# Performance work log

Hardware: AMD Instinct MI355X
Metric: run time of the kernel (lower is better)

## Reference

```python
import jax, jax.numpy as jnp
import numpy as np

EPS = 1e-05
BITW = 8
BITA = 8


def _ste_round(v):
    # round with identity gradient (TF Round->Identity override)
    return v + jax.lax.stop_gradient(jnp.round(v) - v)


def _quantize_overflow(x, bits):
    # tensorlayer _quantize_overflow: linear quantization over [min, max]
    n = 2.0 ** bits - 1.0
    mx = jnp.max(x)
    mn = jnp.min(x)
    step = jax.lax.stop_gradient((mx - mn) / n)
    return _ste_round((x - mn) / step) * step + mn


def _conv2d_same(x, w):
    # x: [N,H,W,C], w: [KH,KW,C,F]
    return jax.lax.conv_general_dilated(
        x, w, window_strides=(1, 1), padding='SAME',
        dimension_numbers=('NHWC', 'HWIO', 'NHWC'))


def setup_inputs() -> dict:
    key = jax.random.key(0)
    k1, k2 = jax.random.split(key)
    x = jax.random.normal(k1, (32, 56, 56, 128), dtype=jnp.float32)
    W = jax.random.normal(k2, (3, 3, 128, 256), dtype=jnp.float32) * 0.02
    gamma = jnp.ones((256,), dtype=jnp.float32)
    beta = jnp.zeros((256,), dtype=jnp.float32)
    return {"x": x, "W": W, "gamma": gamma, "beta": beta}


def reference(x, W, gamma, beta):
    # 1) fake-quantize activations
    xq = _quantize_overflow(x, BITA)
    # 2) full-precision conv to get batch statistics (training path)
    conv_out = _conv2d_same(x, W)  # [N,H,W,F]
    mean = jnp.mean(conv_out, axis=(0, 1, 2))          # [F]
    var = jnp.var(conv_out, axis=(0, 1, 2))            # [F], biased (tf.nn.moments)
    inv_std = 1.0 / jnp.sqrt(var + EPS)                # [F]
    # 3) fold BN into weights/bias
    w_fold = W * (gamma * inv_std)                     # broadcast over [KH,KW,C,F]
    bias_fold = beta - gamma * mean * inv_std          # [F]
    # 4) quantize folded weights, conv with quantized activations
    wq = _quantize_overflow(w_fold, BITW)
    out = _conv2d_same(xq, wq) + bias_fold
    return jax.nn.relu(out)
```

## Files before the change

### kernel.cpp

```cpp
#include <hip/hip_runtime.h>

typedef float f32x4_t __attribute__((ext_vector_type(4)));
typedef __bf16 bf16x8_t __attribute__((ext_vector_type(8)));
typedef unsigned short u16x8_t __attribute__((ext_vector_type(8)));

#define NPIX        100352
#define PIX_PER_IMG 3136
#define PH          58
#define PPIX        3364
#define C_IN        128
#define C_OUT       256
#define NTAPS       9
#define NV4         3211264
#define NWELEM      294912
#define MTILES      392
#define NPADPIX     107648

#define OFF_ENC     0
#define OFF_SCALE   64
#define OFF_BIAS    1152
#define OFF_WT      4096
#define OFF_WQT     593920
#define OFF_PSUM    1183744
#define OFF_PSQ     1986560
#define OFF_XPAD    2789376
#define OFF_XQPAD   30347264

__device__ __forceinline__ unsigned short f2bf(float x) {
  unsigned u = __float_as_uint(x);
  u += 0x7FFFu + ((u >> 16) & 1u);
  return (unsigned short)(u >> 16);
}
__device__ __forceinline__ unsigned encf(float v) {
  unsigned u = __float_as_uint(v);
  return (u & 0x80000000u) ? ~u : (u | 0x80000000u);
}
__device__ __forceinline__ float decf(unsigned e) {
  unsigned u = (e & 0x80000000u) ? (e ^ 0x80000000u) : ~e;
  return __uint_as_float(u);
}
__device__ __forceinline__ void gl_lds16(const void* g, void* l) {
  auto gp = (const __attribute__((address_space(1))) unsigned*)(const unsigned*)g;
  auto lp = (__attribute__((address_space(3))) unsigned*)(unsigned*)l;
  __builtin_amdgcn_global_load_lds(gp, lp, 16, 0, 0);
}
#define SCHED_FENCE() __builtin_amdgcn_sched_barrier(0)

__global__ void kinit(unsigned* enc) {
  enc[0] = 0xFFFFFFFFu;
  enc[1] = 0u;
  enc[2] = 0xFFFFFFFFu;
  enc[3] = 0u;
}

__global__ void kminmax(const float4* __restrict__ x, unsigned* __restrict__ enc) {
  const int tid = blockIdx.x * blockDim.x + threadIdx.x;
  const int stride = gridDim.x * blockDim.x;
  float mn = 3.4e38f, mx = -3.4e38f;
  for (int i = tid; i < NV4; i += stride) {
    float4 v = x[i];
    mn = fminf(mn, fminf(fminf(v.x, v.y), fminf(v.z, v.w)));
    mx = fmaxf(mx, fmaxf(fmaxf(v.x, v.y), fmaxf(v.z, v.w)));
  }
  #pragma unroll
  for (int off = 32; off > 0; off >>= 1) {
    mn = fminf(mn, __shfl_xor(mn, off));
    mx = fmaxf(mx, __shfl_xor(mx, off));
  }
  __shared__ float smn[4], smx[4];
  const int lane = threadIdx.x & 63, w = threadIdx.x >> 6;
  if (lane == 0) { smn[w] = mn; smx[w] = mx; }
  __syncthreads();
  if (threadIdx.x == 0) {
    mn = fminf(fminf(smn[0], smn[1]), fminf(smn[2], smn[3]));
    mx = fmaxf(fmaxf(smx[0], smx[1]), fmaxf(smx[2], smx[3]));
    atomicMin(&enc[0], encf(mn));
    atomicMax(&enc[1], encf(mx));
  }
}

__global__ void kwconv(const float* __restrict__ W, unsigned short* __restrict__ wt) {
  const int idx = blockIdx.x * 256 + threadIdx.x;
  if (idx >= NWELEM) return;
  const int c = idx & 127;
  const int f = (idx >> 7) & 255;
  const int tap = idx >> 15;
  wt[idx] = f2bf(W[(tap * 128 + c) * 256 + f]);
}

__global__ void kwq(const float* __restrict__ W, const float* __restrict__ scale,
                    const unsigned* __restrict__ enc, unsigned short* __restrict__ wqt) {
  const int idx = blockIdx.x * 256 + threadIdx.x;
  if (idx >= NWELEM) return;
  const int c = idx & 127;
  const int f = (idx >> 7) & 255;
  const int tap = idx >> 15;
  const float wmn = decf(enc[2]), wmx = decf(enc[3]);
  const float wstep = (wmx - wmn) / 255.0f;
  const float wrstep = 255.0f / (wmx - wmn);
  const float v = W[(tap * 128 + c) * 256 + f] * scale[f];
  const float q = rintf((v - wmn) * wrstep) * wstep + wmn;
  wqt[idx] = f2bf(q);
}

__global__ void kpadfill(const float* __restrict__ x, const unsigned* __restrict__ enc,
                         unsigned short* __restrict__ xpad, unsigned short* __restrict__ xqpad)
{
  const int tid = blockIdx.x * 256 + threadIdx.x;
  if (tid >= NPADPIX * 16) return;
  const int pp = tid >> 4;
  const int c8 = (tid & 15) << 3;
  const int n = pp / PPIX;
  const int rem = pp - n * PPIX;
  const int hp = rem / PH;
  const int wp = rem - hp * PH;
  u16x8_t vb, vq;
  #pragma unroll
  for (int j = 0; j < 8; ++j) { vb[j] = 0; vq[j] = 0; }
  if (hp >= 1 && hp <= 56 && wp >= 1 && wp <= 56) {
    const float mn = decf(enc[0]), mx = decf(enc[1]);
    const float step = (mx - mn) / 255.0f, rstep = 255.0f / (mx - mn);
    const float* src = x + ((n * PIX_PER_IMG) + (hp - 1) * 56 + (wp - 1)) * C_IN + c8;
    const float4 a = *(const float4*)src;
    const float4 b = *(const float4*)(src + 4);
    const float v[8] = {a.x, a.y, a.z, a.w, b.x, b.y, b.z, b.w};
    #pragma unroll
    for (int j = 0; j < 8; ++j) {
      vb[j] = f2bf(v[j]);
      const float qv = rintf((v[j] - mn) * rstep) * step + mn;
      vq[j] = f2bf(qv);
    }
  }
  *(u16x8_t*)(xpad + pp * C_IN + c8) = vb;
  *(u16x8_t*)(xqpad + pp * C_IN + c8) = vq;
}

template<int STATS>
__global__ __launch_bounds__(512, 4)
void kconv(const unsigned short* __restrict__ xin,
           const unsigned short* __restrict__ wt,
           float* __restrict__ out,
           const float* __restrict__ bias,
           float* __restrict__ psum,
           float* __restrict__ psq)
{
  const int bid = blockIdx.x;
  const int slot = (bid & 7) * 98 + (bid >> 3);
  const int bm = slot >> 1;
  const int bn = slot & 1;

  const int tid = threadIdx.x;
  const int lane = tid & 63;
  const int wid = tid >> 6;
  const int wm = wid >> 1;
  const int wn = wid & 1;
  const int l16 = lane & 15;
  const int rsub = lane >> 4;

  __shared__ __align__(16) unsigned char smem[49152];

  unsigned aoff[2];
  {
    const int arow0 = wid * 8 + (lane >> 3);
    const int pc = lane & 7;
    #pragma unroll
    for (int j = 0; j < 2; ++j) {
      const int row = j * 64 + arow0;
      const int lc = pc ^ (row & 7);
      const int pix = bm * 256 + row + 128 * (lc >> 2);
      const int n = pix / PIX_PER_IMG;
      const int rem = pix - n * PIX_PER_IMG;
      const int hh = rem / 56;
      const int ww = rem - hh * 56;
      aoff[j] = (unsigned)((n * PPIX + hh * PH + ww) * C_IN + (lc & 3) * 8);
    }
  }
  unsigned boff;
  {
    const int row = wid * 8 + (lane >> 3);
    const int pc = lane & 7;
    const int lc = pc ^ (row & 7);
    const int f = bn * 128 + row + 64 * (lc >> 2);
    boff = (unsigned)(f * C_IN + (lc & 3) * 8);
  }

  int a_rd[4], b_rd[4];
  #pragma unroll
  for (int im = 0; im < 4; ++im) {
    const int p = wm * 64 + im * 16 + l16;
    const int row = p & 127, half = p >> 7;
    const int phys = (half * 4 + rsub) ^ (row & 7);
    a_rd[im] = row * 128 + phys * 16;
  }
  #pragma unroll
  for (int in = 0; in < 4; ++in) {
    const int f = wn * 64 + in * 16 + l16;
    const int row = f & 63, half = f >> 6;
    const int phys = (half * 4 + rsub) ^ (row & 7);
    b_rd[in] = row * 128 + phys * 16;
  }

  f32x4_t acc[4][4];
  #pragma unroll
  for (int im = 0; im < 4; ++im)
    #pragma unroll
    for (int in = 0; in < 4; ++in)
      #pragma unroll
      for (int j = 0; j < 4; ++j) acc[im][in][j] = 0.f;

  auto stage = [&](int s) {
    const int tap = s >> 2;
    const int cq = (s & 3) * 32;
    const int kh = tap / 3, kw = tap - kh * 3;
    const unsigned atap = (unsigned)((kh * PH + kw) * C_IN + cq);
    const unsigned btap = (unsigned)(tap * (C_OUT * C_IN) + cq);
    unsigned char* sA = smem + (s & 1) * 24576;
    unsigned char* sB = sA + 16384;
    gl_lds16(xin + atap + aoff[0], sA + wid * 1024);
    gl_lds16(xin + atap + aoff[1], sA + 8192 + wid * 1024);
    gl_lds16(wt + btap + boff, sB + wid * 1024);
  };

  auto compute = [&](int s) {
    const unsigned char* sA = smem + (s & 1) * 24576;
    const unsigned char* sB = sA + 16384;
    bf16x8_t av[4], bv[4];
    #pragma unroll
    for (int im = 0; im < 4; ++im)
      av[im] = *(const bf16x8_t*)(sA + a_rd[im]);
    #pragma unroll
    for (int in = 0; in < 4; ++in)
      bv[in] = *(const bf16x8_t*)(sB + b_rd[in]);
    #pragma unroll
    for (int im = 0; im < 4; ++im)
      #pragma unroll
      for (int in = 0; in < 4; ++in)
        acc[im][in] = __builtin_amdgcn_mfma_f32_16x16x32_bf16(av[im], bv[in], acc[im][in], 0, 0, 0);
  };

  stage(0);
  stage(1);

  #pragma unroll 1
  for (int s = 0; s < 35; ++s) {
    asm volatile("s_waitcnt vmcnt(3)" ::: "memory");
    SCHED_FENCE();
    __builtin_amdgcn_s_barrier();
    SCHED_FENCE();
    compute(s);
    SCHED_FENCE();
    __builtin_amdgcn_s_barrier();
    SCHED_FENCE();
    if (s < 34) stage(s + 2);
  }
  asm volatile("s_waitcnt vmcnt(0)" ::: "memory");
  SCHED_FENCE();
  __builtin_amdgcn_s_barrier();
  SCHED_FENCE();
  compute(35);

  if (STATS) {
    __syncthreads();
    float* sb = (float*)smem;
    #pragma unroll
    for (int in = 0; in < 4; ++in) {
      float s = 0.f, q = 0.f;
      #pragma unroll
      for (int im = 0; im < 4; ++im)
        #pragma unroll
        for (int j = 0; j < 4; ++j) {
          const float v = acc[im][in][j];
          s += v; q += v * v;
        }
      s += __shfl_xor(s, 16); q += __shfl_xor(q, 16);
      s += __shfl_xor(s, 32); q += __shfl_xor(q, 32);
      if (lane < 16) {
        sb[wid * 64 + in * 16 + lane] = s;
        sb[512 + wid * 64 + in * 16 + lane] = q;
      }
    }
    __syncthreads();
    if (tid < 128) {
      const int wn2 = tid >> 6, cl = tid & 63;
      float s = 0.f, q = 0.f;
      #pragma unroll
      for (int wm2 = 0; wm2 < 4; ++wm2) {
        s += sb[(wm2 * 2 + wn2) * 64 + cl];
        q += sb[512 + (wm2 * 2 + wn2) * 64 + cl];
      }
      psum[(bm * 2 + bn) * 128 + tid] = s;
      psq[(bm * 2 + bn) * 128 + tid] = q;
    }
  } else {
    float bval[4];
    #pragma unroll
    for (int in = 0; in < 4; ++in)
      bval[in] = bias[bn * 128 + wn * 64 + in * 16 + l16];
    #pragma unroll
    for (int im = 0; im < 4; ++im) {
      #pragma unroll
      for (int j = 0; j < 4; ++j) {
        const int pix = bm * 256 + wm * 64 + im * 16 + rsub * 4 + j;
        #pragma unroll
        for (int in = 0; in < 4; ++in) {
          const int f = bn * 128 + wn * 64 + in * 16 + l16;
          out[pix * 256 + f] = fmaxf(acc[im][in][j] + bval[in], 0.f);
        }
      }
    }
  }
}

__global__ __launch_bounds__(256)
void kstats(const float* __restrict__ psum, const float* __restrict__ psq,
            const float* __restrict__ gamma, const float* __restrict__ beta,
            float* __restrict__ scale, float* __restrict__ bias)
{
  const int ch = blockIdx.x;
  const int bn = ch >> 7, col = ch & 127;
  float s = 0.f, q = 0.f;
  for (int bm = threadIdx.x; bm < MTILES; bm += 256) {
    s += psum[(bm * 2 + bn) * 128 + col];
    q += psq[(bm * 2 + bn) * 128 + col];
  }
  #pragma unroll
  for (int off = 32; off > 0; off >>= 1) {
    s += __shfl_xor(s, off);
    q += __shfl_xor(q, off);
  }
  __shared__ float ss[4], sq2[4];
  const int lane = threadIdx.x & 63, w = threadIdx.x >> 6;
  if (lane == 0) { ss[w] = s; sq2[w] = q; }
  __syncthreads();
  if (threadIdx.x == 0) {
    s = ss[0] + ss[1] + ss[2] + ss[3];
    q = sq2[0] + sq2[1] + sq2[2] + sq2[3];
    const float inv = 1.0f / (float)NPIX;
    const float mean = s * inv;
    const float var = q * inv - mean * mean;
    const float istd = 1.0f / sqrtf(var + 1e-5f);
    const float g = gamma[ch];
    scale[ch] = g * istd;
    bias[ch] = beta[ch] - g * mean * istd;
  }
}

__global__ __launch_bounds__(256)
void kwmm(const float* __restrict__ W, const float* __restrict__ scale,
          unsigned* __restrict__ enc)
{
  const int idx = blockIdx.x * 256 + threadIdx.x;
  float v = 0.f;
  if (idx < NWELEM) v = W[idx] * scale[idx & 255];
  float mn = v, mx = v;
  #pragma unroll
  for (int off = 32; off > 0; off >>= 1) {
    mn = fminf(mn, __shfl_xor(mn, off));
    mx = fmaxf(mx, __shfl_xor(mx, off));
  }
  __shared__ float rmn[4], rmx[4];
  const int lane = threadIdx.x & 63, w = threadIdx.x >> 6;
  if (lane == 0) { rmn[w] = mn; rmx[w] = mx; }
  __syncthreads();
  if (threadIdx.x == 0) {
    mn = fminf(fminf(rmn[0], rmn[1]), fminf(rmn[2], rmn[3]));
    mx = fmaxf(fmaxf(rmx[0], rmx[1]), fmaxf(rmx[2], rmx[3]));
    atomicMin(&enc[2], encf(mn));
    atomicMax(&enc[3], encf(mx));
  }
}

extern "C" void kernel_launch(void* const* d_in, const int* in_sizes, int n_in,
                              void* d_out, int out_size, void* d_ws, size_t ws_size,
                              hipStream_t stream)
{
  const float* x     = (const float*)d_in[0];
  const float* W     = (const float*)d_in[1];
  const float* gamma = (const float*)d_in[2];
  const float* beta  = (const float*)d_in[3];
  float* out = (float*)d_out;
  char* ws = (char*)d_ws;

  unsigned* enc        = (unsigned*)(ws + OFF_ENC);
  float* scale         = (float*)(ws + OFF_SCALE);
  float* bias          = (float*)(ws + OFF_BIAS);
  unsigned short* Wt   = (unsigned short*)(ws + OFF_WT);
  unsigned short* Wqt  = (unsigned short*)(ws + OFF_WQT);
  float* psum          = (float*)(ws + OFF_PSUM);
  float* psq           = (float*)(ws + OFF_PSQ);
  unsigned short* xpad  = (unsigned short*)(ws + OFF_XPAD);
  unsigned short* xqpad = (unsigned short*)(ws + OFF_XQPAD);

  kinit<<<1, 64, 0, stream>>>(enc);
  kminmax<<<1024, 256, 0, stream>>>((const float4*)x, enc);
  kwconv<<<1152, 256, 0, stream>>>(W, Wt);
  kpadfill<<<6728, 256, 0, stream>>>(x, enc, xpad, xqpad);
  kconv<1><<<784, 512, 0, stream>>>(xpad, Wt, nullptr, nullptr, psum, psq);
  kstats<<<256, 256, 0, stream>>>(psum, psq, gamma, beta, scale, bias);
  kwmm<<<1152, 256, 0, stream>>>(W, scale, enc);
  kwq<<<1152, 256, 0, stream>>>(W, scale, enc, Wqt);
  kconv<0><<<784, 512, 0, stream>>>(xqpad, Wqt, out, bias, nullptr, nullptr);
}
```

Before: 236.7 us.

## Run quantized conv on int8 MFMA with zero-point correction terms

The second convolution now stores quantized activations and folded weights as signed int8 codes and accumulates with the i8 MFMA instruction. The affine quantization offsets are restored in the epilogue using per-pixel box sums of activation codes and per-tap, per-filter weight code sums, with border pixels handled explicitly. This halves the activation and weight bytes loaded and doubles the K per MFMA, which cuts loop iterations. The cost is extra small kernels (box filter, j1 reduction) and a heavier epilogue with a per-pixel divide and a border-tap loop, plus float rounding differences in the reconstructed affine terms.

```diff
diff --git a/kernel.cpp b/kernel.cpp
--- a/kernel.cpp
+++ b/kernel.cpp
@@ -1,6 +1,7 @@
 #include <hip/hip_runtime.h>
 
 typedef float f32x4_t __attribute__((ext_vector_type(4)));
+typedef int i32x4_t __attribute__((ext_vector_type(4)));
 typedef __bf16 bf16x8_t __attribute__((ext_vector_type(8)));
 typedef unsigned short u16x8_t __attribute__((ext_vector_type(8)));
 
@@ -19,12 +20,16 @@
 #define OFF_ENC     0
 #define OFF_SCALE   64
 #define OFF_BIAS    1152
-#define OFF_WT      4096
-#define OFF_WQT     593920
-#define OFF_PSUM    1183744
-#define OFF_PSQ     1986560
-#define OFF_XPAD    2789376
-#define OFF_XQPAD   30347264
+#define OFF_J1TAP   2176
+#define OFF_J1ALL   11392
+#define OFF_WT      16384
+#define OFF_WQT8    606208
+#define OFF_PSUM    901120
+#define OFF_PSQ     1302528
+#define OFF_K1      1703936
+#define OFF_SCP     2105344
+#define OFF_XPAD    2535936
+#define OFF_XQ8     30093824
 
 __device__ __forceinline__ unsigned short f2bf(float x) {
   unsigned u = __float_as_uint(x);
@@ -47,10 +52,8 @@
 #define SCHED_FENCE() __builtin_amdgcn_sched_barrier(0)
 
 __global__ void kinit(unsigned* enc) {
-  enc[0] = 0xFFFFFFFFu;
-  enc[1] = 0u;
-  enc[2] = 0xFFFFFFFFu;
-  enc[3] = 0u;
+  enc[0] = 0xFFFFFFFFu; enc[1] = 0u;
+  enc[2] = 0xFFFFFFFFu; enc[3] = 0u;
 }
 
 __global__ void kminmax(const float4* __restrict__ x, unsigned* __restrict__ enc) {
@@ -88,23 +91,41 @@
   wt[idx] = f2bf(W[(tap * 128 + c) * 256 + f]);
 }
 
-__global__ void kwq(const float* __restrict__ W, const float* __restrict__ scale,
-                    const unsigned* __restrict__ enc, unsigned short* __restrict__ wqt) {
+__global__ __launch_bounds__(256)
+void kwq(const float* __restrict__ W, const float* __restrict__ scale,
+         const unsigned* __restrict__ enc, signed char* __restrict__ wq8,
+         float* __restrict__ j1tap) {
   const int idx = blockIdx.x * 256 + threadIdx.x;
-  if (idx >= NWELEM) return;
   const int c = idx & 127;
   const int f = (idx >> 7) & 255;
   const int tap = idx >> 15;
   const float wmn = decf(enc[2]), wmx = decf(enc[3]);
-  const float wstep = (wmx - wmn) / 255.0f;
   const float wrstep = 255.0f / (wmx - wmn);
   const float v = W[(tap * 128 + c) * 256 + f] * scale[f];
-  const float q = rintf((v - wmn) * wrstep) * wstep + wmn;
-  wqt[idx] = f2bf(q);
+  const int code = (int)rintf((v - wmn) * wrstep) - 128;
+  wq8[idx] = (signed char)code;
+  float p = (float)code;
+  #pragma unroll
+  for (int off = 32; off > 0; off >>= 1) p += __shfl_xor(p, off);
+  __shared__ float sb[4];
+  const int lane = threadIdx.x & 63, wv = threadIdx.x >> 6;
+  if (lane == 0) sb[wv] = p;
+  __syncthreads();
+  if (threadIdx.x == 0)   j1tap[tap * 256 + f] = sb[0] + sb[1];
+  if (threadIdx.x == 128) j1tap[tap * 256 + f] = sb[2] + sb[3];
+}
+
+__global__ void kjall(const float* __restrict__ j1tap, float* __restrict__ j1all) {
+  const int f = threadIdx.x;
+  float s = 0.f;
+  #pragma unroll
+  for (int t = 0; t < 9; ++t) s += j1tap[t * 256 + f];
+  j1all[f] = s;
 }
 
 __global__ void kpadfill(const float* __restrict__ x, const unsigned* __restrict__ enc,
-                         unsigned short* __restrict__ xpad, unsigned short* __restrict__ xqpad)
+                         unsigned short* __restrict__ xpad, signed char* __restrict__ xq8,
+                         float* __restrict__ scp)
 {
   const int tid = blockIdx.x * 256 + threadIdx.x;
   if (tid >= NPADPIX * 16) return;
@@ -114,12 +135,14 @@
   const int rem = pp - n * PPIX;
   const int hp = rem / PH;
   const int wp = rem - hp * PH;
-  u16x8_t vb, vq;
-  #pragma unroll
-  for (int j = 0; j < 8; ++j) { vb[j] = 0; vq[j] = 0; }
+  u16x8_t vb;
+  int codes[8];
+  #pragma unroll
+  for (int j = 0; j < 8; ++j) { vb[j] = 0; codes[j] = 0; }
+  float csum = 0.f;
   if (hp >= 1 && hp <= 56 && wp >= 1 && wp <= 56) {
     const float mn = decf(enc[0]), mx = decf(enc[1]);
-    const float step = (mx - mn) / 255.0f, rstep = 255.0f / (mx - mn);
+    const float rstep = 255.0f / (mx - mn);
     const float* src = x + ((n * PIX_PER_IMG) + (hp - 1) * 56 + (wp - 1)) * C_IN + c8;
     const float4 a = *(const float4*)src;
     const float4 b = *(const float4*)(src + 4);
@@ -127,22 +150,46 @@
     #pragma unroll
     for (int j = 0; j < 8; ++j) {
       vb[j] = f2bf(v[j]);
-      const float qv = rintf((v[j] - mn) * rstep) * step + mn;
-      vq[j] = f2bf(qv);
+      const int k = (int)rintf((v[j] - mn) * rstep);
+      codes[j] = k - 128;
+      csum += (float)(k - 128);
     }
   }
   *(u16x8_t*)(xpad + pp * C_IN + c8) = vb;
-  *(u16x8_t*)(xqpad + pp * C_IN + c8) = vq;
-}
-
-template<int STATS>
+  unsigned long long pk = 0;
+  #pragma unroll
+  for (int j = 0; j < 8; ++j)
+    pk |= ((unsigned long long)(unsigned char)(signed char)codes[j]) << (8 * j);
+  *(unsigned long long*)(xq8 + pp * C_IN + c8) = pk;
+  csum += __shfl_xor(csum, 1, 16);
+  csum += __shfl_xor(csum, 2, 16);
+  csum += __shfl_xor(csum, 4, 16);
+  csum += __shfl_xor(csum, 8, 16);
+  if ((threadIdx.x & 15) == 0) scp[pp] = csum;
+}
+
+__global__ __launch_bounds__(256)
+void kbox(const float* __restrict__ scp, float* __restrict__ k1) {
+  const int pix = blockIdx.x * 256 + threadIdx.x;
+  if (pix >= NPIX) return;
+  const int n = pix / PIX_PER_IMG;
+  const int rem = pix - n * PIX_PER_IMG;
+  const int h = rem / 56;
+  const int w = rem - h * 56;
+  const float* base = scp + n * PPIX + h * PH + w;
+  float s = 0.f;
+  #pragma unroll
+  for (int dh = 0; dh < 3; ++dh)
+    #pragma unroll
+    for (int dw = 0; dw < 3; ++dw)
+      s += base[dh * PH + dw];
+  k1[pix] = s;
+}
+
 __global__ __launch_bounds__(512, 4)
-void kconv(const unsigned short* __restrict__ xin,
-           const unsigned short* __restrict__ wt,
-           float* __restrict__ out,
-           const float* __restrict__ bias,
-           float* __restrict__ psum,
-           float* __restrict__ psq)
+void kconvS(const unsigned short* __restrict__ xin,
+            const unsigned short* __restrict__ wt,
+            float* __restrict__ psum, float* __restrict__ psq)
 {
   const int bid = blockIdx.x;
   const int slot = (bid & 7) * 98 + (bid >> 3);
@@ -226,11 +273,9 @@
     const unsigned char* sB = sA + 16384;
     bf16x8_t av[4], bv[4];
     #pragma unroll
-    for (int im = 0; im < 4; ++im)
-      av[im] = *(const bf16x8_t*)(sA + a_rd[im]);
-    #pragma unroll
-    for (int in = 0; in < 4; ++in)
-      bv[in] = *(const bf16x8_t*)(sB + b_rd[in]);
+    for (int im = 0; im < 4; ++im) av[im] = *(const bf16x8_t*)(sA + a_rd[im]);
+    #pragma unroll
+    for (int in = 0; in < 4; ++in) bv[in] = *(const bf16x8_t*)(sB + b_rd[in]);
     #pragma unroll
     for (int im = 0; im < 4; ++im)
       #pragma unroll
@@ -238,9 +283,7 @@
         acc[im][in] = __builtin_amdgcn_mfma_f32_16x16x32_bf16(av[im], bv[in], acc[im][in], 0, 0, 0);
   };
 
-  stage(0);
-  stage(1);
-
+  stage(0); stage(1);
   #pragma unroll 1
   for (int s = 0; s < 35; ++s) {
     asm volatile("s_waitcnt vmcnt(3)" ::: "memory");
@@ -259,53 +302,208 @@
   SCHED_FENCE();
   compute(35);
 
-  if (STATS) {
-    __syncthreads();
-    float* sb = (float*)smem;
-    #pragma unroll
-    for (int in = 0; in < 4; ++in) {
-      float s = 0.f, q = 0.f;
-      #pragma unroll
-      for (int im = 0; im < 4; ++im)
-        #pragma unroll
-        for (int j = 0; j < 4; ++j) {
-          const float v = acc[im][in][j];
-          s += v; q += v * v;
-        }
-      s += __shfl_xor(s, 16); q += __shfl_xor(q, 16);
-      s += __shfl_xor(s, 32); q += __shfl_xor(q, 32);
-      if (lane < 16) {
-        sb[wid * 64 + in * 16 + lane] = s;
-        sb[512 + wid * 64 + in * 16 + lane] = q;
-      }
-    }
-    __syncthreads();
-    if (tid < 128) {
-      const int wn2 = tid >> 6, cl = tid & 63;
-      float s = 0.f, q = 0.f;
-      #pragma unroll
-      for (int wm2 = 0; wm2 < 4; ++wm2) {
-        s += sb[(wm2 * 2 + wn2) * 64 + cl];
-        q += sb[512 + (wm2 * 2 + wn2) * 64 + cl];
-      }
-      psum[(bm * 2 + bn) * 128 + tid] = s;
-      psq[(bm * 2 + bn) * 128 + tid] = q;
-    }
-  } else {
-    float bval[4];
-    #pragma unroll
-    for (int in = 0; in < 4; ++in)
-      bval[in] = bias[bn * 128 + wn * 64 + in * 16 + l16];
-    #pragma unroll
-    for (int im = 0; im < 4; ++im) {
+  __syncthreads();
+  float* sb = (float*)smem;
+  #pragma unroll
+  for (int in = 0; in < 4; ++in) {
+    float s = 0.f, q = 0.f;
+    #pragma unroll
+    for (int im = 0; im < 4; ++im)
       #pragma unroll
       for (int j = 0; j < 4; ++j) {
-        const int pix = bm * 256 + wm * 64 + im * 16 + rsub * 4 + j;
-        #pragma unroll
-        for (int in = 0; in < 4; ++in) {
-          const int f = bn * 128 + wn * 64 + in * 16 + l16;
-          out[pix * 256 + f] = fmaxf(acc[im][in][j] + bval[in], 0.f);
+        const float v = acc[im][in][j];
+        s += v; q += v * v;
+      }
+    s += __shfl_xor(s, 16); q += __shfl_xor(q, 16);
+    s += __shfl_xor(s, 32); q += __shfl_xor(q, 32);
+    if (lane < 16) {
+      sb[wid * 64 + in * 16 + lane] = s;
+      sb[512 + wid * 64 + in * 16 + lane] = q;
+    }
+  }
+  __syncthreads();
+  if (tid < 128) {
+    const int wn2 = tid >> 6, cl = tid & 63;
+    float s = 0.f, q = 0.f;
+    #pragma unroll
+    for (int wm2 = 0; wm2 < 4; ++wm2) {
+      s += sb[(wm2 * 2 + wn2) * 64 + cl];
+      q += sb[512 + (wm2 * 2 + wn2) * 64 + cl];
+    }
+    psum[(bm * 2 + bn) * 128 + tid] = s;
+    psq[(bm * 2 + bn) * 128 + tid] = q;
+  }
+}
+
+__global__ __launch_bounds__(512, 4)
+void kconv2(const signed char* __restrict__ xq8,
+            const signed char* __restrict__ wq8,
+            float* __restrict__ out,
+            const float* __restrict__ bias,
+            const float* __restrict__ k1,
+            const float* __restrict__ j1tap,
+            const float* __restrict__ j1all,
+            const unsigned* __restrict__ enc)
+{
+  const int bid = blockIdx.x;
+  const int slot = (bid & 7) * 98 + (bid >> 3);
+  const int bm = slot >> 1;
+  const int bn = slot & 1;
+
+  const int tid = threadIdx.x;
+  const int lane = tid & 63;
+  const int wid = tid >> 6;
+  const int wm = wid >> 1;
+  const int wn = wid & 1;
+  const int l16 = lane & 15;
+  const int rsub = lane >> 4;
+
+  __shared__ __align__(16) unsigned char smem[49152];
+
+  unsigned aoff[2];
+  {
+    const int arow0 = wid * 8 + (lane >> 3);
+    const int pc = lane & 7;
+    #pragma unroll
+    for (int j = 0; j < 2; ++j) {
+      const int row = j * 64 + arow0;
+      const int lc = pc ^ (row & 7);
+      const int pix = bm * 256 + row + 128 * (lc >> 2);
+      const int n = pix / PIX_PER_IMG;
+      const int rem = pix - n * PIX_PER_IMG;
+      const int hh = rem / 56;
+      const int ww = rem - hh * 56;
+      aoff[j] = (unsigned)((n * PPIX + hh * PH + ww) * 128 + (lc & 3) * 16);
+    }
+  }
+  unsigned boff;
+  {
+    const int row = wid * 8 + (lane >> 3);
+    const int pc = lane & 7;
+    const int lc = pc ^ (row & 7);
+    const int f = bn * 128 + row + 64 * (lc >> 2);
+    boff = (unsigned)(f * 128 + (lc & 3) * 16);
+  }
+
+  int a_rd[4], b_rd[4];
+  #pragma unroll
+  for (int im = 0; im < 4; ++im) {
+    const int p = wm * 64 + im * 16 + l16;
+    const int row = p & 127, half = p >> 7;
+    const int phys = (half * 4 + rsub) ^ (row & 7);
+    a_rd[im] = row * 128 + phys * 16;
+  }
+  #pragma unroll
+  for (int in = 0; in < 4; ++in) {
+    const int f = wn * 64 + in * 16 + l16;
+    const int row = f & 63, half = f >> 6;
+    const int phys = (half * 4 + rsub) ^ (row & 7);
+    b_rd[in] = row * 128 + phys * 16;
+  }
+
+  i32x4_t acc[4][4];
+  #pragma unroll
+  for (int im = 0; im < 4; ++im)
+    #pragma unroll
+    for (int in = 0; in < 4; ++in)
+      #pragma unroll
+      for (int j = 0; j < 4; ++j) acc[im][in][j] = 0;
+
+  auto stage = [&](int s) {
+    const int tap = s >> 1;
+    const int ch64 = (s & 1) << 6;
+    const int kh = tap / 3, kw = tap - kh * 3;
+    const unsigned atap = (unsigned)((kh * PH + kw) * 128 + ch64);
+    const unsigned btap = (unsigned)(tap * (C_OUT * 128) + ch64);
+    unsigned char* sA = smem + (s & 1) * 24576;
+    unsigned char* sB = sA + 16384;
+    gl_lds16(xq8 + atap + aoff[0], sA + wid * 1024);
+    gl_lds16(xq8 + atap + aoff[1], sA + 8192 + wid * 1024);
+    gl_lds16(wq8 + btap + boff, sB + wid * 1024);
+  };
+
+  auto compute = [&](int s) {
+    const unsigned char* sA = smem + (s & 1) * 24576;
+    const unsigned char* sB = sA + 16384;
+    i32x4_t av[4], bv[4];
+    #pragma unroll
+    for (int im = 0; im < 4; ++im) av[im] = *(const i32x4_t*)(sA + a_rd[im]);
+    #pragma unroll
+    for (int in = 0; in < 4; ++in) bv[in] = *(const i32x4_t*)(sB + b_rd[in]);
+    #pragma unroll
+    for (int im = 0; im < 4; ++im)
+      #pragma unroll
+      for (int in = 0; in < 4; ++in)
+        acc[im][in] = __builtin_amdgcn_mfma_i32_16x16x64_i8(av[im], bv[in], acc[im][in], 0, 0, 0);
+  };
+
+  stage(0); stage(1);
+  #pragma unroll 1
+  for (int s = 0; s < 17; ++s) {
+    asm volatile("s_waitcnt vmcnt(3)" ::: "memory");
+    SCHED_FENCE();
+    __builtin_amdgcn_s_barrier();
+    SCHED_FENCE();
+    compute(s);
+    SCHED_FENCE();
+    __builtin_amdgcn_s_barrier();
+    SCHED_FENCE();
+    if (s < 16) stage(s + 2);
+  }
+  asm volatile("s_waitcnt vmcnt(0)" ::: "memory");
+  SCHED_FENCE();
+  __builtin_amdgcn_s_barrier();
+  SCHED_FENCE();
+  compute(17);
+
+  const float xmn = decf(enc[0]), xmx = decf(enc[1]);
+  const float sx = (xmx - xmn) / 255.0f;
+  const float wmn = decf(enc[2]), wmx = decf(enc[3]);
+  const float sw = (wmx - wmn) / 255.0f;
+  const float ap = xmn / sx + 128.0f;
+  const float bp = wmn / sw + 128.0f;
+  const float sxw = sx * sw;
+
+  float biasv[4], j1av[4];
+  int fidx[4];
+  #pragma unroll
+  for (int in = 0; in < 4; ++in) {
+    fidx[in] = bn * 128 + wn * 64 + in * 16 + l16;
+    biasv[in] = bias[fidx[in]];
+    j1av[in] = j1all[fidx[in]];
+  }
+
+  #pragma unroll
+  for (int im = 0; im < 4; ++im) {
+    const int pixbase = bm * 256 + wm * 64 + im * 16 + rsub * 4;
+    const float4 k1v = *(const float4*)(k1 + pixbase);
+    #pragma unroll
+    for (int j = 0; j < 4; ++j) {
+      const int pix = pixbase + j;
+      const int n = pix / PIX_PER_IMG;
+      const int rem = pix - n * PIX_PER_IMG;
+      const int h = rem / 56;
+      const int w = rem - h * 56;
+      const int khl = (h == 0) ? 1 : 0;
+      const int khh = (h == 55) ? 1 : 2;
+      const int kwl = (w == 0) ? 1 : 0;
+      const int kwh = (w == 55) ? 1 : 2;
+      const int ntap = (khh - khl + 1) * (kwh - kwl + 1);
+      const float k1s = (j == 0) ? k1v.x : (j == 1) ? k1v.y : (j == 2) ? k1v.z : k1v.w;
+      const float base_corr = bp * k1s + ap * bp * (float)(ntap << 7);
+      #pragma unroll
+      for (int in = 0; in < 4; ++in) {
+        float jv;
+        if (ntap == 9) {
+          jv = j1av[in];
+        } else {
+          jv = 0.f;
+          for (int kh = khl; kh <= khh; ++kh)
+            for (int kw = kwl; kw <= kwh; ++kw)
+              jv += j1tap[(kh * 3 + kw) * 256 + fidx[in]];
         }
+        const float r = sxw * ((float)acc[im][in][j] + base_corr + ap * jv) + biasv[in];
+        out[pix * 256 + fidx[in]] = fmaxf(r, 0.f);
       }
     }
   }
@@ -384,20 +582,26 @@
   unsigned* enc        = (unsigned*)(ws + OFF_ENC);
   float* scale         = (float*)(ws + OFF_SCALE);
   float* bias          = (float*)(ws + OFF_BIAS);
+  float* j1tap         = (float*)(ws + OFF_J1TAP);
+  float* j1all         = (float*)(ws + OFF_J1ALL);
   unsigned short* Wt   = (unsigned short*)(ws + OFF_WT);
-  unsigned short* Wqt  = (unsigned short*)(ws + OFF_WQT);
+  signed char* wq8     = (signed char*)(ws + OFF_WQT8);
   float* psum          = (float*)(ws + OFF_PSUM);
   float* psq           = (float*)(ws + OFF_PSQ);
-  unsigned short* xpad  = (unsigned short*)(ws + OFF_XPAD);
-  unsigned short* xqpad = (unsigned short*)(ws + OFF_XQPAD);
+  float* k1            = (float*)(ws + OFF_K1);
+  float* scp           = (float*)(ws + OFF_SCP);
+  unsigned short* xpad = (unsigned short*)(ws + OFF_XPAD);
+  signed char* xq8     = (signed char*)(ws + OFF_XQ8);
 
   kinit<<<1, 64, 0, stream>>>(enc);
   kminmax<<<1024, 256, 0, stream>>>((const float4*)x, enc);
   kwconv<<<1152, 256, 0, stream>>>(W, Wt);
-  kpadfill<<<6728, 256, 0, stream>>>(x, enc, xpad, xqpad);
-  kconv<1><<<784, 512, 0, stream>>>(xpad, Wt, nullptr, nullptr, psum, psq);
+  kpadfill<<<6728, 256, 0, stream>>>(x, enc, xpad, xq8, scp);
+  kbox<<<392, 256, 0, stream>>>(scp, k1);
+  kconvS<<<784, 512, 0, stream>>>(xpad, Wt, psum, psq);
   kstats<<<256, 256, 0, stream>>>(psum, psq, gamma, beta, scale, bias);
   kwmm<<<1152, 256, 0, stream>>>(W, scale, enc);
-  kwq<<<1152, 256, 0, stream>>>(W, scale, enc, Wqt);
-  kconv<0><<<784, 512, 0, stream>>>(xqpad, Wqt, out, bias, nullptr, nullptr);
-}
+  kwq<<<1152, 256, 0, stream>>>(W, scale, enc, wq8, j1tap);
+  kjall<<<1, 256, 0, stream>>>(j1tap, j1all);
+  kconv2<<<784, 512, 0, stream>>>(xq8, wq8, out, bias, k1, j1tap, j1all, enc);
+}
```

After: 254.0 us. 1.07x slower.

## Triple-buffer conv K-loop with single barrier and rotate tap order per block

Applied to the files above, without the earlier changes.

The conv main loop moves from double to triple LDS buffering. Each iteration now needs one barrier instead of two, and the next stage's global-to-LDS loads are issued before the MFMA compute instead of after it. Odd blocks also start the K loop at a rotated tap offset, which spreads concurrent global reads of the same weight and activation slices. LDS per block grows from 48KB to 72KB, which may lower occupancy under the 512-thread, 4-blocks launch bounds.

```diff
diff --git a/kernel.cpp b/kernel.cpp
--- a/kernel.cpp
+++ b/kernel.cpp
@@ -10,7 +10,6 @@
 #define PPIX        3364
 #define C_IN        128
 #define C_OUT       256
-#define NTAPS       9
 #define NV4         3211264
 #define NWELEM      294912
 #define MTILES      392
@@ -47,10 +46,8 @@
 #define SCHED_FENCE() __builtin_amdgcn_sched_barrier(0)
 
 __global__ void kinit(unsigned* enc) {
-  enc[0] = 0xFFFFFFFFu;
-  enc[1] = 0u;
-  enc[2] = 0xFFFFFFFFu;
-  enc[3] = 0u;
+  enc[0] = 0xFFFFFFFFu; enc[1] = 0u;
+  enc[2] = 0xFFFFFFFFu; enc[3] = 0u;
 }
 
 __global__ void kminmax(const float4* __restrict__ x, unsigned* __restrict__ enc) {
@@ -148,6 +145,7 @@
   const int slot = (bid & 7) * 98 + (bid >> 3);
   const int bm = slot >> 1;
   const int bn = slot & 1;
+  const int rot = (bid & 1) * 18;
 
   const int tid = threadIdx.x;
   const int lane = tid & 63;
@@ -157,7 +155,7 @@
   const int l16 = lane & 15;
   const int rsub = lane >> 4;
 
-  __shared__ __align__(16) unsigned char smem[49152];
+  __shared__ __align__(16) unsigned char smem[73728];
 
   unsigned aoff[2];
   {
@@ -209,12 +207,13 @@
       for (int j = 0; j < 4; ++j) acc[im][in][j] = 0.f;
 
   auto stage = [&](int s) {
-    const int tap = s >> 2;
-    const int cq = (s & 3) * 32;
+    int pt = s + rot; if (pt >= 36) pt -= 36;
+    const int tap = pt >> 2;
+    const int cq = (pt & 3) * 32;
     const int kh = tap / 3, kw = tap - kh * 3;
     const unsigned atap = (unsigned)((kh * PH + kw) * C_IN + cq);
     const unsigned btap = (unsigned)(tap * (C_OUT * C_IN) + cq);
-    unsigned char* sA = smem + (s & 1) * 24576;
+    unsigned char* sA = smem + (s % 3) * 24576;
     unsigned char* sB = sA + 16384;
     gl_lds16(xin + atap + aoff[0], sA + wid * 1024);
     gl_lds16(xin + atap + aoff[1], sA + 8192 + wid * 1024);
@@ -222,15 +221,13 @@
   };
 
   auto compute = [&](int s) {
-    const unsigned char* sA = smem + (s & 1) * 24576;
+    const unsigned char* sA = smem + (s % 3) * 24576;
     const unsigned char* sB = sA + 16384;
     bf16x8_t av[4], bv[4];
     #pragma unroll
-    for (int im = 0; im < 4; ++im)
-      av[im] = *(const bf16x8_t*)(sA + a_rd[im]);
-    #pragma unroll
-    for (int in = 0; in < 4; ++in)
-      bv[in] = *(const bf16x8_t*)(sB + b_rd[in]);
+    for (int im = 0; im < 4; ++im) av[im] = *(const bf16x8_t*)(sA + a_rd[im]);
+    #pragma unroll
+    for (int in = 0; in < 4; ++in) bv[in] = *(const bf16x8_t*)(sB + b_rd[in]);
     #pragma unroll
     for (int im = 0; im < 4; ++im)
       #pragma unroll
@@ -242,22 +239,15 @@
   stage(1);
 
   #pragma unroll 1
-  for (int s = 0; s < 35; ++s) {
-    asm volatile("s_waitcnt vmcnt(3)" ::: "memory");
-    SCHED_FENCE();
-    __builtin_amdgcn_s_barrier();
-    SCHED_FENCE();
-    compute(s);
+  for (int s = 0; s < 36; ++s) {
+    if (s < 35) asm volatile("s_waitcnt vmcnt(3)" ::: "memory");
+    else        asm volatile("s_waitcnt vmcnt(0)" ::: "memory");
     SCHED_FENCE();
     __builtin_amdgcn_s_barrier();
     SCHED_FENCE();
     if (s < 34) stage(s + 2);
-  }
-  asm volatile("s_waitcnt vmcnt(0)" ::: "memory");
-  SCHED_FENCE();
-  __builtin_amdgcn_s_barrier();
-  SCHED_FENCE();
-  compute(35);
+    compute(s);
+  }
 
   if (STATS) {
     __syncthreads();
```

Result: no change. 238.0 us (+0.5%).

## Shrink conv block tile to 128x128 with 4 waves and fold weight cast into padfill

Applied to the files above, without the earlier changes.

The implicit-GEMM conv kernel moves from 256x128 tiles with 8 waves to 128x128 tiles with 4 waves. Shared memory drops to 32 KB and the grid doubles to 1568 blocks, so more blocks can be resident and the tail is more even. The cost is less reuse of the weight tile per block and more global traffic, plus more per-tile partial stats for kstats to reduce. Separately, the bf16 weight-cast kernel is merged into the pad-fill launch as extra blocks to save one kernel launch.

```diff
diff --git a/kernel.cpp b/kernel.cpp
--- a/kernel.cpp
+++ b/kernel.cpp
@@ -10,10 +10,9 @@
 #define PPIX        3364
 #define C_IN        128
 #define C_OUT       256
-#define NTAPS       9
 #define NV4         3211264
 #define NWELEM      294912
-#define MTILES      392
+#define MT128       784
 #define NPADPIX     107648
 
 #define OFF_ENC     0
@@ -47,10 +46,8 @@
 #define SCHED_FENCE() __builtin_amdgcn_sched_barrier(0)
 
 __global__ void kinit(unsigned* enc) {
-  enc[0] = 0xFFFFFFFFu;
-  enc[1] = 0u;
-  enc[2] = 0xFFFFFFFFu;
-  enc[3] = 0u;
+  enc[0] = 0xFFFFFFFFu; enc[1] = 0u;
+  enc[2] = 0xFFFFFFFFu; enc[3] = 0u;
 }
 
 __global__ void kminmax(const float4* __restrict__ x, unsigned* __restrict__ enc) {
@@ -77,15 +74,6 @@
     atomicMin(&enc[0], encf(mn));
     atomicMax(&enc[1], encf(mx));
   }
-}
-
-__global__ void kwconv(const float* __restrict__ W, unsigned short* __restrict__ wt) {
-  const int idx = blockIdx.x * 256 + threadIdx.x;
-  if (idx >= NWELEM) return;
-  const int c = idx & 127;
-  const int f = (idx >> 7) & 255;
-  const int tap = idx >> 15;
-  wt[idx] = f2bf(W[(tap * 128 + c) * 256 + f]);
 }
 
 __global__ void kwq(const float* __restrict__ W, const float* __restrict__ scale,
@@ -104,8 +92,19 @@
 }
 
 __global__ void kpadfill(const float* __restrict__ x, const unsigned* __restrict__ enc,
-                         unsigned short* __restrict__ xpad, unsigned short* __restrict__ xqpad)
-{
+                         unsigned short* __restrict__ xpad, unsigned short* __restrict__ xqpad,
+                         const float* __restrict__ W, unsigned short* __restrict__ wtt)
+{
+  if (blockIdx.x >= 6728) {
+    const int idx = (blockIdx.x - 6728) * 256 + threadIdx.x;
+    if (idx < NWELEM) {
+      const int c = idx & 127;
+      const int f = (idx >> 7) & 255;
+      const int tap = idx >> 15;
+      wtt[idx] = f2bf(W[(tap * 128 + c) * 256 + f]);
+    }
+    return;
+  }
   const int tid = blockIdx.x * 256 + threadIdx.x;
   if (tid >= NPADPIX * 16) return;
   const int pp = tid >> 4;
@@ -136,7 +135,7 @@
 }
 
 template<int STATS>
-__global__ __launch_bounds__(512, 4)
+__global__ __launch_bounds__(256, 4)
 void kconv(const unsigned short* __restrict__ xin,
            const unsigned short* __restrict__ wt,
            float* __restrict__ out,
@@ -145,7 +144,7 @@
            float* __restrict__ psq)
 {
   const int bid = blockIdx.x;
-  const int slot = (bid & 7) * 98 + (bid >> 3);
+  const int slot = (bid & 7) * 196 + (bid >> 3);
   const int bm = slot >> 1;
   const int bn = slot & 1;
 
@@ -157,38 +156,31 @@
   const int l16 = lane & 15;
   const int rsub = lane >> 4;
 
-  __shared__ __align__(16) unsigned char smem[49152];
-
-  unsigned aoff[2];
+  __shared__ __align__(16) unsigned char smem[32768];
+
+  unsigned aoff[2], boff[2];
   {
-    const int arow0 = wid * 8 + (lane >> 3);
-    const int pc = lane & 7;
+    const int pc = tid & 7;
     #pragma unroll
     for (int j = 0; j < 2; ++j) {
-      const int row = j * 64 + arow0;
+      const int row = j * 32 + (tid >> 3);
       const int lc = pc ^ (row & 7);
-      const int pix = bm * 256 + row + 128 * (lc >> 2);
+      const int pix = bm * 128 + row + 64 * (lc >> 2);
       const int n = pix / PIX_PER_IMG;
       const int rem = pix - n * PIX_PER_IMG;
       const int hh = rem / 56;
       const int ww = rem - hh * 56;
       aoff[j] = (unsigned)((n * PPIX + hh * PH + ww) * C_IN + (lc & 3) * 8);
-    }
-  }
-  unsigned boff;
-  {
-    const int row = wid * 8 + (lane >> 3);
-    const int pc = lane & 7;
-    const int lc = pc ^ (row & 7);
-    const int f = bn * 128 + row + 64 * (lc >> 2);
-    boff = (unsigned)(f * C_IN + (lc & 3) * 8);
+      const int f = bn * 128 + row + 64 * (lc >> 2);
+      boff[j] = (unsigned)(f * C_IN + (lc & 3) * 8);
+    }
   }
 
   int a_rd[4], b_rd[4];
   #pragma unroll
   for (int im = 0; im < 4; ++im) {
     const int p = wm * 64 + im * 16 + l16;
-    const int row = p & 127, half = p >> 7;
+    const int row = p & 63, half = p >> 6;
     const int phys = (half * 4 + rsub) ^ (row & 7);
     a_rd[im] = row * 128 + phys * 16;
   }
@@ -214,23 +206,22 @@
     const int kh = tap / 3, kw = tap - kh * 3;
     const unsigned atap = (unsigned)((kh * PH + kw) * C_IN + cq);
     const unsigned btap = (unsigned)(tap * (C_OUT * C_IN) + cq);
-    unsigned char* sA = smem + (s & 1) * 24576;
-    unsigned char* sB = sA + 16384;
+    unsigned char* sA = smem + (s & 1) * 16384;
+    unsigned char* sB = sA + 8192;
     gl_lds16(xin + atap + aoff[0], sA + wid * 1024);
-    gl_lds16(xin + atap + aoff[1], sA + 8192 + wid * 1024);
-    gl_lds16(wt + btap + boff, sB + wid * 1024);
+    gl_lds16(xin + atap + aoff[1], sA + 4096 + wid * 1024);
+    gl_lds16(wt + btap + boff[0], sB + wid * 1024);
+    gl_lds16(wt + btap + boff[1], sB + 4096 + wid * 1024);
   };
 
   auto compute = [&](int s) {
-    const unsigned char* sA = smem + (s & 1) * 24576;
-    const unsigned char* sB = sA + 16384;
+    const unsigned char* sA = smem + (s & 1) * 16384;
+    const unsigned char* sB = sA + 8192;
     bf16x8_t av[4], bv[4];
     #pragma unroll
-    for (int im = 0; im < 4; ++im)
-      av[im] = *(const bf16x8_t*)(sA + a_rd[im]);
-    #pragma unroll
-    for (int in = 0; in < 4; ++in)
-      bv[in] = *(const bf16x8_t*)(sB + b_rd[in]);
+    for (int im = 0; im < 4; ++im) av[im] = *(const bf16x8_t*)(sA + a_rd[im]);
+    #pragma unroll
+    for (int in = 0; in < 4; ++in) bv[in] = *(const bf16x8_t*)(sB + b_rd[in]);
     #pragma unroll
     for (int im = 0; im < 4; ++im)
       #pragma unroll
@@ -243,7 +234,7 @@
 
   #pragma unroll 1
   for (int s = 0; s < 35; ++s) {
-    asm volatile("s_waitcnt vmcnt(3)" ::: "memory");
+    asm volatile("s_waitcnt vmcnt(4)" ::: "memory");
     SCHED_FENCE();
     __builtin_amdgcn_s_barrier();
     SCHED_FENCE();
@@ -276,18 +267,14 @@
       s += __shfl_xor(s, 32); q += __shfl_xor(q, 32);
       if (lane < 16) {
         sb[wid * 64 + in * 16 + lane] = s;
-        sb[512 + wid * 64 + in * 16 + lane] = q;
+        sb[256 + wid * 64 + in * 16 + lane] = q;
       }
     }
     __syncthreads();
     if (tid < 128) {
       const int wn2 = tid >> 6, cl = tid & 63;
-      float s = 0.f, q = 0.f;
-      #pragma unroll
-      for (int wm2 = 0; wm2 < 4; ++wm2) {
-        s += sb[(wm2 * 2 + wn2) * 64 + cl];
-        q += sb[512 + (wm2 * 2 + wn2) * 64 + cl];
-      }
+      const float s = sb[wn2 * 64 + cl] + sb[(2 + wn2) * 64 + cl];
+      const float q = sb[256 + wn2 * 64 + cl] + sb[256 + (2 + wn2) * 64 + cl];
       psum[(bm * 2 + bn) * 128 + tid] = s;
       psq[(bm * 2 + bn) * 128 + tid] = q;
     }
@@ -300,7 +287,7 @@
     for (int im = 0; im < 4; ++im) {
       #pragma unroll
       for (int j = 0; j < 4; ++j) {
-        const int pix = bm * 256 + wm * 64 + im * 16 + rsub * 4 + j;
+        const int pix = bm * 128 + wm * 64 + im * 16 + rsub * 4 + j;
         #pragma unroll
         for (int in = 0; in < 4; ++in) {
           const int f = bn * 128 + wn * 64 + in * 16 + l16;
@@ -319,7 +306,7 @@
   const int ch = blockIdx.x;
   const int bn = ch >> 7, col = ch & 127;
   float s = 0.f, q = 0.f;
-  for (int bm = threadIdx.x; bm < MTILES; bm += 256) {
+  for (int bm = threadIdx.x; bm < MT128; bm += 256) {
     s += psum[(bm * 2 + bn) * 128 + col];
     q += psq[(bm * 2 + bn) * 128 + col];
   }
@@ -393,11 +380,10 @@
 
   kinit<<<1, 64, 0, stream>>>(enc);
   kminmax<<<1024, 256, 0, stream>>>((const float4*)x, enc);
-  kwconv<<<1152, 256, 0, stream>>>(W, Wt);
-  kpadfill<<<6728, 256, 0, stream>>>(x, enc, xpad, xqpad);
-  kconv<1><<<784, 512, 0, stream>>>(xpad, Wt, nullptr, nullptr, psum, psq);
+  kpadfill<<<7880, 256, 0, stream>>>(x, enc, xpad, xqpad, W, Wt);
+  kconv<1><<<1568, 256, 0, stream>>>(xpad, Wt, nullptr, nullptr, psum, psq);
   kstats<<<256, 256, 0, stream>>>(psum, psq, gamma, beta, scale, bias);
   kwmm<<<1152, 256, 0, stream>>>(W, scale, enc);
   kwq<<<1152, 256, 0, stream>>>(W, scale, enc, Wqt);
-  kconv<0><<<784, 512, 0, stream>>>(xqpad, Wqt, out, bias, nullptr, nullptr);
-}
+  kconv<0><<<1568, 256, 0, stream>>>(xqpad, Wqt, out, bias, nullptr, nullptr);
+}
```

Result: slower. 241.7 us (+2.1%).
